# Kernel optimization log

Measured on AMD Instinct MI355X. Metric: run time of the kernel, lower is better.

Reference implementation:

```python
import jax, jax.numpy as jnp
import numpy as np

M = 16                      # multiplicity of each irrep block
INV3 = 1.0 / np.sqrt(3.0)   # w3j(1,1,0) component-normalized
INV2 = 1.0 / np.sqrt(2.0)   # w3j(1,1,1) component-normalized
A0 = 1.0 / np.sqrt(2.0 * M) # fan-in norm for 0e outputs (2 paths x mul 16)
A1 = 1.0 / np.sqrt(3.0 * M) # fan-in norm for 1o outputs (3 paths x mul 16)


def setup_inputs() -> dict:
    E, N, ED, HID = 100000, 10000, 32, 128
    WNUM = 2 * M * (2 * M) + 3 * M * M  # 1792 per-edge TP weights
    ks = jax.random.split(jax.random.key(0), 10)
    return {
        "dst": jax.random.randint(ks[0], (E,), 0, N),
        "x_src": jax.random.normal(ks[1], (E, 4 * M), jnp.float32),   # 16x0e+16x1o
        "x_dst": jax.random.normal(ks[2], (N, 4 * M), jnp.float32),
        "sh": jax.random.normal(ks[3], (E, 4), jnp.float32),          # 1x0e+1x1o
        "edge_attr": jax.random.normal(ks[4], (E, ED), jnp.float32),
        "We1": jax.random.normal(ks[5], (ED, HID), jnp.float32) / np.sqrt(ED),
        "be1": jnp.zeros((HID,), jnp.float32),
        "We2": jax.random.normal(ks[6], (HID, WNUM), jnp.float32) / np.sqrt(HID),
        "be2": jnp.zeros((WNUM,), jnp.float32),
        "Wr0": jax.random.normal(ks[7], (M, 2 * M), jnp.float32),     # 16x0e -> 32x0e
        "Wr1": jax.random.normal(ks[8], (M, M), jnp.float32),         # 16x1o -> 16x1o
    }


def _forward(dst, x_src, x_dst, sh, edge_attr, We1, be1, We2, be2, Wr0, Wr1):
    E = x_src.shape[0]
    N = x_dst.shape[0]
    o0 = 2 * M  # 32x0e tp output (scalars + gates)

    # edge MLP -> per-edge tensor-product weights [E, 1792]
    w = jax.nn.relu(edge_attr @ We1 + be1) @ We2 + be2
    i = 0
    w_ss = w[:, i:i + M * o0].reshape(E, M, o0); i += M * o0   # 0e x 0e -> 0e
    w_vv0 = w[:, i:i + M * o0].reshape(E, M, o0); i += M * o0  # 1o x 1o -> 0e
    w_sv = w[:, i:i + M * M].reshape(E, M, M); i += M * M      # 0e x 1o -> 1o
    w_vs = w[:, i:i + M * M].reshape(E, M, M); i += M * M      # 1o x 0e -> 1o
    w_vv1 = w[:, i:i + M * M].reshape(E, M, M)                 # 1o x 1o -> 1o

    s1 = x_src[:, :M]                       # [E, 16]
    v1 = x_src[:, M:].reshape(E, M, 3)      # [E, 16, 3]
    s2 = sh[:, 0]                           # [E]
    v2 = sh[:, 1:4]                         # [E, 3]

    # fully-connected tensor product with per-edge weights
    out0 = A0 * (jnp.einsum('em,emo->eo', s1 * s2[:, None], w_ss)
                 + INV3 * jnp.einsum('emc,ec,emo->eo', v1, v2, w_vv0))  # [E, 32]
    cross = jnp.cross(v1, v2[:, None, :])   # [E, 16, 3]
    out1 = A1 * (jnp.einsum('em,ec,emo->eoc', s1, v2, w_sv)
                 + jnp.einsum('emc,e,emo->eoc', v1, s2, w_vs)
                 + INV2 * jnp.einsum('emc,emo->eoc', cross, w_vv1))     # [E, 16, 3]
    msg = jnp.concatenate([out0, out1.reshape(E, -1)], axis=1)          # [E, 80]

    # scatter-mean over destination nodes
    ssum = jax.ops.segment_sum(msg, dst, num_segments=N)
    cnt = jax.ops.segment_sum(jnp.ones((E,), msg.dtype), dst, num_segments=N)
    msg = ssum / jnp.maximum(cnt, 1.0)[:, None]                          # [N, 80]

    # residual equivariant linear on x_dst
    sd = x_dst[:, :M]
    vd = x_dst[:, M:].reshape(N, M, 3)
    res0 = (sd @ Wr0) / np.sqrt(M)                                       # [N, 32]
    res1 = jnp.einsum('nmc,mo->noc', vd, Wr1) / np.sqrt(M)               # [N, 16, 3]
    msg = msg + jnp.concatenate([res0, res1.reshape(N, -1)], axis=1)

    # gate nonlinearity: relu(scalars), sigmoid(gates) * gated vectors
    scalars = jax.nn.relu(msg[:, :M])
    gates = jax.nn.sigmoid(msg[:, M:2 * M])
    gated = msg[:, 2 * M:].reshape(N, M, 3) * gates[:, :, None]
    return jnp.concatenate([scalars, gated.reshape(N, -1)], axis=1)      # [N, 64]


def reference(dst, x_src, x_dst, sh, edge_attr, We1, be1, We2, be2, Wr0, Wr1):
    return _forward(dst, x_src, x_dst, sh, edge_attr, We1, be1, We2, be2, Wr0, Wr1)
```

## Files before the change

### kernel.cpp

```cpp
#include <hip/hip_runtime.h>
#include <math.h>

#define WNUM 1792
#define HID 128

#define INV3C 0.5773502691896258f
#define INV2C 0.7071067811865476f
#define A0C   0.17677669529663687f
#define A1C   0.14433756729740643f

typedef short bf8 __attribute__((ext_vector_type(8)));
typedef _Float16 f16x8 __attribute__((ext_vector_type(8)));
typedef _Float16 f16x4 __attribute__((ext_vector_type(4)));
typedef float f32x4 __attribute__((ext_vector_type(4)));

__device__ inline unsigned short f2bf(float f) {
  union { float f; unsigned u; } v; v.f = f;
  unsigned r = v.u + 0x7FFFu + ((v.u >> 16) & 1u);
  return (unsigned short)(r >> 16);
}
__device__ inline float bf2f(unsigned short h) {
  union { unsigned u; float f; } v; v.u = ((unsigned)h) << 16;
  return v.f;
}
__device__ inline float wscale(int t) {
  if (t < 32) return A0C;
  if (t < 64) return A0C * INV3C;
  if (t < 96) return A1C;
  return A1C * INV2C;
}

__global__ __launch_bounds__(256) void prep_kernel(
    const float* __restrict__ We1, const float* __restrict__ We2,
    const float* __restrict__ be2,
    unsigned short* __restrict__ we1x, _Float16* __restrict__ we2h,
    float* __restrict__ be2p)
{
  int i = blockIdx.x * 256 + threadIdx.x;
  if (i < 28672) {
    int t = i >> 8, c = (i >> 6) & 3, lane = i & 63;
    int quad = lane >> 4, l15 = lane & 15;
    int col = t * 16 + l15;
    float sc = wscale(t);
    f16x8 v;
    #pragma unroll
    for (int j = 0; j < 8; ++j) {
      int k = c * 32 + quad * 8 + j;
      v[j] = (_Float16)(We2[(size_t)k * WNUM + col] * sc);
    }
    *(f16x8*)(we2h + (size_t)t * 2048 + c * 512 + lane * 8) = v;
  } else if (i < 29184) {
    int q = i - 28672;
    int c1 = q >> 6, lane = q & 63;
    int quad = lane >> 4, l15 = lane & 15;
    int col = c1 * 16 + l15;
    bf8 hh, ll;
    #pragma unroll
    for (int j = 0; j < 8; ++j) {
      int k = quad * 8 + j;
      float v = We1[k * HID + col];
      unsigned short hi = f2bf(v);
      hh[j] = (short)hi;
      ll[j] = (short)f2bf(v - bf2f(hi));
    }
    *(bf8*)(we1x + c1 * 1024 + lane * 8) = hh;
    *(bf8*)(we1x + c1 * 1024 + 512 + lane * 8) = ll;
  } else if (i < 30976) {
    int q = i - 29184;
    int t = q >> 4, l16 = q & 15;
    be2p[(t >> 1) * 32 + l16 * 2 + (t & 1)] = be2[q] * wscale(t);
  }
}

__device__ inline void chains2(const f16x8* a0, const f16x8* a1,
    f16x8 b0, f16x8 b1, f16x8 b2, f16x8 b3,
    f16x8 b4, f16x8 b5, f16x8 b6, f16x8 b7,
    float2 bias, f32x4* wa, f32x4* wb)
{
  f32x4 ca0 = {bias.x, bias.x, bias.x, bias.x};
  f32x4 cb0 = {bias.y, bias.y, bias.y, bias.y};
  f32x4 ca1 = ca0, cb1 = cb0;
  ca0 = __builtin_amdgcn_mfma_f32_16x16x32_f16(a0[0], b0, ca0, 0, 0, 0);
  cb0 = __builtin_amdgcn_mfma_f32_16x16x32_f16(a0[0], b4, cb0, 0, 0, 0);
  ca1 = __builtin_amdgcn_mfma_f32_16x16x32_f16(a1[0], b0, ca1, 0, 0, 0);
  cb1 = __builtin_amdgcn_mfma_f32_16x16x32_f16(a1[0], b4, cb1, 0, 0, 0);
  ca0 = __builtin_amdgcn_mfma_f32_16x16x32_f16(a0[1], b1, ca0, 0, 0, 0);
  cb0 = __builtin_amdgcn_mfma_f32_16x16x32_f16(a0[1], b5, cb0, 0, 0, 0);
  ca1 = __builtin_amdgcn_mfma_f32_16x16x32_f16(a1[1], b1, ca1, 0, 0, 0);
  cb1 = __builtin_amdgcn_mfma_f32_16x16x32_f16(a1[1], b5, cb1, 0, 0, 0);
  ca0 = __builtin_amdgcn_mfma_f32_16x16x32_f16(a0[2], b2, ca0, 0, 0, 0);
  cb0 = __builtin_amdgcn_mfma_f32_16x16x32_f16(a0[2], b6, cb0, 0, 0, 0);
  ca1 = __builtin_amdgcn_mfma_f32_16x16x32_f16(a1[2], b2, ca1, 0, 0, 0);
  cb1 = __builtin_amdgcn_mfma_f32_16x16x32_f16(a1[2], b6, cb1, 0, 0, 0);
  ca0 = __builtin_amdgcn_mfma_f32_16x16x32_f16(a0[3], b3, ca0, 0, 0, 0);
  cb0 = __builtin_amdgcn_mfma_f32_16x16x32_f16(a0[3], b7, cb0, 0, 0, 0);
  ca1 = __builtin_amdgcn_mfma_f32_16x16x32_f16(a1[3], b3, ca1, 0, 0, 0);
  cb1 = __builtin_amdgcn_mfma_f32_16x16x32_f16(a1[3], b7, cb1, 0, 0, 0);
  wa[0] = ca0; wb[0] = cb0; wa[1] = ca1; wb[1] = cb1;
}

#define LOADB(P) \
  f16x8 b0, b1, b2, b3, b4, b5, b6, b7; float2 bias2; \
  { const _Float16* q_ = bW + (size_t)(P) * 4096; \
    b0 = *(const f16x8*)(q_);        b1 = *(const f16x8*)(q_ + 512); \
    b2 = *(const f16x8*)(q_ + 1024); b3 = *(const f16x8*)(q_ + 1536); \
    b4 = *(const f16x8*)(q_ + 2048); b5 = *(const f16x8*)(q_ + 2560); \
    b6 = *(const f16x8*)(q_ + 3072); b7 = *(const f16x8*)(q_ + 3584); \
    bias2 = *(const float2*)(bp + (P) * 32); }

__global__ __launch_bounds__(128, 2) void edge_kernel(
    const float* __restrict__ ea, const float* __restrict__ xsrc,
    const float* __restrict__ sh, const int* __restrict__ dst,
    const float* __restrict__ be1,
    const unsigned short* __restrict__ we1x, const _Float16* __restrict__ we2h,
    const float* __restrict__ be2p,
    float* __restrict__ accn, float* __restrict__ cnt, int E)
{
  const int lane = threadIdx.x & 63;
  const int w    = threadIdx.x >> 6;
  const int quad = lane >> 4;
  const int l16  = lane & 15;
  const int eb   = (blockIdx.x * 2 + w) * 32;

  __shared__ _Float16 h_s[2][32][136];
  __shared__ _Float16 fss_s[2][16][32];
  __shared__ _Float16 fvv_s[2][16][32];
  __shared__ _Float16 s1h_s[2][16][32];
  __shared__ _Float16 v1h_s[2][16][3][32];
  __shared__ float4 vq_s[2][32];

  {
    int e2 = lane >> 1, mg = lane & 1;
    int ge = eb + e2;
    if (ge < E) {
      const float* xp = xsrc + (size_t)ge * 64;
      float4 sq0 = *(const float4*)(xp + mg * 8);
      float4 sq1 = *(const float4*)(xp + mg * 8 + 4);
      float s1a[8] = {sq0.x,sq0.y,sq0.z,sq0.w,sq1.x,sq1.y,sq1.z,sq1.w};
      const float* vp = xp + 16 + mg * 24;
      float la[24];
      #pragma unroll
      for (int qv = 0; qv < 6; ++qv) {
        float4 t = *(const float4*)(vp + qv * 4);
        la[qv*4+0] = t.x; la[qv*4+1] = t.y; la[qv*4+2] = t.z; la[qv*4+3] = t.w;
      }
      float4 shq = *(const float4*)(sh + (size_t)ge * 4);
      float s2 = shq.x, v2x = shq.y, v2y = shq.z, v2z = shq.w;
      #pragma unroll
      for (int mi = 0; mi < 8; ++mi) {
        int m = mg * 8 + mi;
        float v1x = la[mi*3], v1y = la[mi*3+1], v1z = la[mi*3+2];
        fss_s[w][m][e2] = (_Float16)(s1a[mi] * s2);
        fvv_s[w][m][e2] = (_Float16)(v1x*v2x + v1y*v2y + v1z*v2z);
        s1h_s[w][m][e2] = (_Float16)s1a[mi];
        v1h_s[w][m][0][e2] = (_Float16)v1x;
        v1h_s[w][m][1][e2] = (_Float16)v1y;
        v1h_s[w][m][2][e2] = (_Float16)v1z;
      }
      if (mg == 0) vq_s[w][e2] = make_float4(v2x, v2y, v2z, s2);
    } else {
      #pragma unroll
      for (int mi = 0; mi < 8; ++mi) {
        int m = mg * 8 + mi;
        fss_s[w][m][e2] = (_Float16)0.f;
        fvv_s[w][m][e2] = (_Float16)0.f;
        s1h_s[w][m][e2] = (_Float16)0.f;
        v1h_s[w][m][0][e2] = (_Float16)0.f;
        v1h_s[w][m][1][e2] = (_Float16)0.f;
        v1h_s[w][m][2][e2] = (_Float16)0.f;
      }
      if (mg == 0) vq_s[w][e2] = make_float4(0,0,0,0);
    }
  }

  {
    bf8 ah[2], al[2];
    #pragma unroll
    for (int g = 0; g < 2; ++g) {
      int gea = eb + g * 16 + l16; if (gea > E - 1) gea = E - 1;
      const float* ep = ea + (size_t)gea * 32 + quad * 8;
      float4 p0 = *(const float4*)ep;
      float4 p1 = *(const float4*)(ep + 4);
      float pv[8] = {p0.x,p0.y,p0.z,p0.w,p1.x,p1.y,p1.z,p1.w};
      #pragma unroll
      for (int j = 0; j < 8; ++j) {
        unsigned short hi = f2bf(pv[j]);
        ah[g][j] = (short)hi;
        al[g][j] = (short)f2bf(pv[j] - bf2f(hi));
      }
    }
    const unsigned short* wb1 = we1x + lane * 8;
    #pragma unroll 2
    for (int c = 0; c < 8; ++c) {
      bf8 bh = *(const bf8*)(wb1 + c * 1024);
      bf8 bl = *(const bf8*)(wb1 + c * 1024 + 512);
      float bias = be1[c * 16 + l16];
      #pragma unroll
      for (int g = 0; g < 2; ++g) {
        f32x4 hc = {bias, bias, bias, bias};
        hc = __builtin_amdgcn_mfma_f32_16x16x32_bf16(al[g], bh, hc, 0, 0, 0);
        hc = __builtin_amdgcn_mfma_f32_16x16x32_bf16(ah[g], bl, hc, 0, 0, 0);
        hc = __builtin_amdgcn_mfma_f32_16x16x32_bf16(ah[g], bh, hc, 0, 0, 0);
        #pragma unroll
        for (int r = 0; r < 4; ++r)
          h_s[w][g * 16 + quad * 4 + r][c * 16 + l16] = (_Float16)fmaxf(hc[r], 0.f);
      }
    }
  }
  __syncthreads();

  f16x8 af[2][4];
  #pragma unroll
  for (int g = 0; g < 2; ++g)
    #pragma unroll
    for (int ch = 0; ch < 4; ++ch)
      af[g][ch] = *(const f16x8*)&h_s[w][g * 16 + l16][ch * 32 + quad * 8];

  const _Float16* bW = we2h + lane * 8;
  const float* bp = be2p + l16 * 2;

  float m0a[2][4] = {{0,0,0,0},{0,0,0,0}}, m0b[2][4] = {{0,0,0,0},{0,0,0,0}};

  #pragma unroll 1
  for (int i = 0; i < 16; ++i) {
    LOADB(i)
    f32x4 wa[2], wb[2];
    chains2(af[0], af[1], b0,b1,b2,b3,b4,b5,b6,b7, bias2, wa, wb);
    #pragma unroll
    for (int g = 0; g < 2; ++g) {
      f16x4 fv = *(const f16x4*)&fss_s[w][i][g * 16 + quad * 4];
      #pragma unroll
      for (int r = 0; r < 4; ++r) {
        float f = (float)fv[r];
        m0a[g][r] = fmaf(wa[g][r], f, m0a[g][r]);
        m0b[g][r] = fmaf(wb[g][r], f, m0b[g][r]);
      }
    }
  }

  #pragma unroll 1
  for (int i = 0; i < 16; ++i) {
    LOADB(16 + i)
    f32x4 wa[2], wb[2];
    chains2(af[0], af[1], b0,b1,b2,b3,b4,b5,b6,b7, bias2, wa, wb);
    #pragma unroll
    for (int g = 0; g < 2; ++g) {
      f16x4 fv = *(const f16x4*)&fvv_s[w][i][g * 16 + quad * 4];
      #pragma unroll
      for (int r = 0; r < 4; ++r) {
        float f = (float)fv[r];
        m0a[g][r] = fmaf(wa[g][r], f, m0a[g][r]);
        m0b[g][r] = fmaf(wb[g][r], f, m0b[g][r]);
      }
    }
  }

  #pragma unroll
  for (int g = 0; g < 2; ++g)
    #pragma unroll
    for (int r = 0; r < 4; ++r) {
      int ge = eb + g * 16 + quad * 4 + r;
      if (ge < E) {
        float* ap = accn + (size_t)dst[ge] * 80;
        atomicAdd(ap + l16,      m0a[g][r]);
        atomicAdd(ap + 16 + l16, m0b[g][r]);
      }
    }
  if (lane < 32) {
    int ge = eb + lane;
    if (ge < E) atomicAdd(cnt + dst[ge], 1.0f);
  }

  float sg[2][4] = {{0,0,0,0},{0,0,0,0}};
  #pragma unroll 1
  for (int i = 0; i < 8; ++i) {
    LOADB(32 + i)
    f32x4 wa[2], wb[2];
    chains2(af[0], af[1], b0,b1,b2,b3,b4,b5,b6,b7, bias2, wa, wb);
    #pragma unroll
    for (int g = 0; g < 2; ++g) {
      f16x4 sA = *(const f16x4*)&s1h_s[w][2*i][g * 16 + quad * 4];
      f16x4 sB = *(const f16x4*)&s1h_s[w][2*i + 1][g * 16 + quad * 4];
      #pragma unroll
      for (int r = 0; r < 4; ++r)
        sg[g][r] = fmaf(wb[g][r], (float)sB[r], fmaf(wa[g][r], (float)sA[r], sg[g][r]));
    }
  }
  float4 vq[2][4];
  #pragma unroll
  for (int g = 0; g < 2; ++g)
    #pragma unroll
    for (int r = 0; r < 4; ++r) vq[g][r] = vq_s[w][g * 16 + quad * 4 + r];

  float m1x[2][4], m1y[2][4], m1z[2][4];
  #pragma unroll
  for (int g = 0; g < 2; ++g)
    #pragma unroll
    for (int r = 0; r < 4; ++r) {
      m1x[g][r] = sg[g][r] * vq[g][r].x;
      m1y[g][r] = sg[g][r] * vq[g][r].y;
      m1z[g][r] = sg[g][r] * vq[g][r].z;
    }

  {
    float ux[2][4] = {{0,0,0,0},{0,0,0,0}}, uy[2][4] = {{0,0,0,0},{0,0,0,0}},
          uz[2][4] = {{0,0,0,0},{0,0,0,0}};
    #pragma unroll 1
    for (int i = 0; i < 8; ++i) {
      LOADB(40 + i)
      f32x4 wa[2], wb[2];
      chains2(af[0], af[1], b0,b1,b2,b3,b4,b5,b6,b7, bias2, wa, wb);
      #pragma unroll
      for (int g = 0; g < 2; ++g) {
        f16x4 xA = *(const f16x4*)&v1h_s[w][2*i][0][g*16 + quad*4];
        f16x4 xB = *(const f16x4*)&v1h_s[w][2*i+1][0][g*16 + quad*4];
        f16x4 yA = *(const f16x4*)&v1h_s[w][2*i][1][g*16 + quad*4];
        f16x4 yB = *(const f16x4*)&v1h_s[w][2*i+1][1][g*16 + quad*4];
        f16x4 zA = *(const f16x4*)&v1h_s[w][2*i][2][g*16 + quad*4];
        f16x4 zB = *(const f16x4*)&v1h_s[w][2*i+1][2][g*16 + quad*4];
        #pragma unroll
        for (int r = 0; r < 4; ++r) {
          ux[g][r] = fmaf(wb[g][r], (float)xB[r], fmaf(wa[g][r], (float)xA[r], ux[g][r]));
          uy[g][r] = fmaf(wb[g][r], (float)yB[r], fmaf(wa[g][r], (float)yA[r], uy[g][r]));
          uz[g][r] = fmaf(wb[g][r], (float)zB[r], fmaf(wa[g][r], (float)zA[r], uz[g][r]));
        }
      }
    }
    #pragma unroll
    for (int g = 0; g < 2; ++g)
      #pragma unroll
      for (int r = 0; r < 4; ++r) {
        m1x[g][r] = fmaf(vq[g][r].w, ux[g][r], m1x[g][r]);
        m1y[g][r] = fmaf(vq[g][r].w, uy[g][r], m1y[g][r]);
        m1z[g][r] = fmaf(vq[g][r].w, uz[g][r], m1z[g][r]);
      }
  }

  {
    float ux[2][4] = {{0,0,0,0},{0,0,0,0}}, uy[2][4] = {{0,0,0,0},{0,0,0,0}},
          uz[2][4] = {{0,0,0,0},{0,0,0,0}};
    #pragma unroll 1
    for (int i = 0; i < 8; ++i) {
      LOADB(48 + i)
      f32x4 wa[2], wb[2];
      chains2(af[0], af[1], b0,b1,b2,b3,b4,b5,b6,b7, bias2, wa, wb);
      #pragma unroll
      for (int g = 0; g < 2; ++g) {
        f16x4 xA = *(const f16x4*)&v1h_s[w][2*i][0][g*16 + quad*4];
        f16x4 xB = *(const f16x4*)&v1h_s[w][2*i+1][0][g*16 + quad*4];
        f16x4 yA = *(const f16x4*)&v1h_s[w][2*i][1][g*16 + quad*4];
        f16x4 yB = *(const f16x4*)&v1h_s[w][2*i+1][1][g*16 + quad*4];
        f16x4 zA = *(const f16x4*)&v1h_s[w][2*i][2][g*16 + quad*4];
        f16x4 zB = *(const f16x4*)&v1h_s[w][2*i+1][2][g*16 + quad*4];
        #pragma unroll
        for (int r = 0; r < 4; ++r) {
          ux[g][r] = fmaf(wb[g][r], (float)xB[r], fmaf(wa[g][r], (float)xA[r], ux[g][r]));
          uy[g][r] = fmaf(wb[g][r], (float)yB[r], fmaf(wa[g][r], (float)yA[r], uy[g][r]));
          uz[g][r] = fmaf(wb[g][r], (float)zB[r], fmaf(wa[g][r], (float)zA[r], uz[g][r]));
        }
      }
    }
    #pragma unroll
    for (int g = 0; g < 2; ++g)
      #pragma unroll
      for (int r = 0; r < 4; ++r) {
        m1x[g][r] = fmaf(uy[g][r], vq[g][r].z, m1x[g][r]);
        m1x[g][r] = fmaf(-uz[g][r], vq[g][r].y, m1x[g][r]);
        m1y[g][r] = fmaf(uz[g][r], vq[g][r].x, m1y[g][r]);
        m1y[g][r] = fmaf(-ux[g][r], vq[g][r].z, m1y[g][r]);
        m1z[g][r] = fmaf(ux[g][r], vq[g][r].y, m1z[g][r]);
        m1z[g][r] = fmaf(-uy[g][r], vq[g][r].x, m1z[g][r]);
      }
  }

  #pragma unroll
  for (int g = 0; g < 2; ++g)
    #pragma unroll
    for (int r = 0; r < 4; ++r) {
      int ge = eb + g * 16 + quad * 4 + r;
      if (ge < E) {
        float* ap = accn + (size_t)dst[ge] * 80;
        atomicAdd(ap + 32 + l16*3 + 0, m1x[g][r]);
        atomicAdd(ap + 32 + l16*3 + 1, m1y[g][r]);
        atomicAdd(ap + 32 + l16*3 + 2, m1z[g][r]);
      }
    }
}

__global__ __launch_bounds__(256) void node_kernel(
    const float* __restrict__ accn, const float* __restrict__ cnt,
    const float* __restrict__ xdst, const float* __restrict__ Wr0,
    const float* __restrict__ Wr1, float* __restrict__ out, int N)
{
  int idx = blockIdx.x * 256 + threadIdx.x;
  int n = idx >> 6, j = idx & 63;
  if (n >= N) return;
  float inv = 1.0f / fmaxf(cnt[n], 1.0f);
  const float* ap = accn + (size_t)n * 80;
  const float* xd = xdst + (size_t)n * 64;
  float* op = out + (size_t)n * 64;
  if (j < 16) {
    float s = 0.f;
    #pragma unroll
    for (int m = 0; m < 16; ++m) s = fmaf(xd[m], Wr0[m * 32 + j], s);
    op[j] = fmaxf(ap[j] * inv + 0.25f * s, 0.f);
  } else {
    int jj = j - 16;
    int o = (jj * 86) >> 8;
    int c = jj - o * 3;
    float tg = 0.f, v = 0.f;
    #pragma unroll
    for (int m = 0; m < 16; ++m) {
      tg = fmaf(xd[m], Wr0[m * 32 + 16 + o], tg);
      v  = fmaf(xd[16 + m * 3 + c], Wr1[m * 16 + o], v);
    }
    float g = 1.0f / (1.0f + expf(-(ap[16 + o] * inv + 0.25f * tg)));
    op[16 + jj] = (ap[32 + jj] * inv + 0.25f * v) * g;
  }
}

extern "C" void kernel_launch(void* const* d_in, const int* in_sizes, int n_in,
                              void* d_out, int out_size, void* d_ws, size_t ws_size,
                              hipStream_t stream)
{
  const int*   dst  = (const int*)d_in[0];
  const float* xsrc = (const float*)d_in[1];
  const float* xdst = (const float*)d_in[2];
  const float* sh   = (const float*)d_in[3];
  const float* ea   = (const float*)d_in[4];
  const float* We1  = (const float*)d_in[5];
  const float* be1  = (const float*)d_in[6];
  const float* We2  = (const float*)d_in[7];
  const float* be2  = (const float*)d_in[8];
  const float* Wr0  = (const float*)d_in[9];
  const float* Wr1  = (const float*)d_in[10];
  const int E = in_sizes[0];
  const int N = in_sizes[2] / 64;

  char* ws = (char*)d_ws;
  _Float16* we2h = (_Float16*)ws;
  unsigned short* we1x = (unsigned short*)(ws + 458752);
  float* be2p = (float*)(ws + 475136);
  float* accn = (float*)(ws + 482560);
  float* cnt  = (float*)(ws + 482560 + (size_t)N * 320);

  hipMemsetAsync(accn, 0, (size_t)N * 320 + (size_t)N * 4, stream);

  prep_kernel<<<(30976 + 255) / 256, 256, 0, stream>>>(We1, We2, be2, we1x, we2h, be2p);
  edge_kernel<<<(E + 63) / 64, 128, 0, stream>>>(ea, xsrc, sh, dst, be1,
      we1x, we2h, be2p, accn, cnt, E);
  node_kernel<<<((size_t)N * 64 + 255) / 256, 256, 0, stream>>>(accn, cnt, xdst, Wr0, Wr1,
      (float*)d_out, N);
}
```

Baseline: 239.1 us.

## Stage We2 tiles into LDS with double-buffered global_load_lds shared by four waves

Each wave previously loaded its own copy of the per-edge MLP second-layer weight tiles straight from global memory. The block now has four waves, which cooperatively stream each 4096-element fp16 tile into a double-buffered LDS area with global_load_lds, prefetching the next tile while the current one is used. This cuts global/L2 traffic for the weights by sharing them across waves. In exchange it adds a block-wide barrier per tile and raises LDS use per block, which may lower occupancy.

After: 232.6 us. -2.7%, faster.

```diff
diff --git a/kernel.cpp b/kernel.cpp
--- a/kernel.cpp
+++ b/kernel.cpp
@@ -99,16 +99,17 @@
   wa[0] = ca0; wb[0] = cb0; wa[1] = ca1; wb[1] = cb1;
 }
 
-#define LOADB(P) \
-  f16x8 b0, b1, b2, b3, b4, b5, b6, b7; float2 bias2; \
-  { const _Float16* q_ = bW + (size_t)(P) * 4096; \
-    b0 = *(const f16x8*)(q_);        b1 = *(const f16x8*)(q_ + 512); \
-    b2 = *(const f16x8*)(q_ + 1024); b3 = *(const f16x8*)(q_ + 1536); \
-    b4 = *(const f16x8*)(q_ + 2048); b5 = *(const f16x8*)(q_ + 2560); \
-    b6 = *(const f16x8*)(q_ + 3072); b7 = *(const f16x8*)(q_ + 3584); \
-    bias2 = *(const float2*)(bp + (P) * 32); }
-
-__global__ __launch_bounds__(128, 2) void edge_kernel(
+#define LOADB_LDS(BASE) \
+  f16x8 b0 = *(const f16x8*)((BASE)); \
+  f16x8 b1 = *(const f16x8*)((BASE) + 512); \
+  f16x8 b2 = *(const f16x8*)((BASE) + 1024); \
+  f16x8 b3 = *(const f16x8*)((BASE) + 1536); \
+  f16x8 b4 = *(const f16x8*)((BASE) + 2048); \
+  f16x8 b5 = *(const f16x8*)((BASE) + 2560); \
+  f16x8 b6 = *(const f16x8*)((BASE) + 3072); \
+  f16x8 b7 = *(const f16x8*)((BASE) + 3584);
+
+__global__ __launch_bounds__(256, 2) void edge_kernel(
     const float* __restrict__ ea, const float* __restrict__ xsrc,
     const float* __restrict__ sh, const int* __restrict__ dst,
     const float* __restrict__ be1,
@@ -120,14 +121,25 @@
   const int w    = threadIdx.x >> 6;
   const int quad = lane >> 4;
   const int l16  = lane & 15;
-  const int eb   = (blockIdx.x * 2 + w) * 32;
-
-  __shared__ _Float16 h_s[2][32][136];
-  __shared__ _Float16 fss_s[2][16][32];
-  __shared__ _Float16 fvv_s[2][16][32];
-  __shared__ _Float16 s1h_s[2][16][32];
-  __shared__ _Float16 v1h_s[2][16][3][32];
-  __shared__ float4 vq_s[2][32];
+  const int eb   = (blockIdx.x * 4 + w) * 32;
+
+  __shared__ _Float16 Bsm[2][4096];
+  __shared__ _Float16 h_s[4][32][136];
+  __shared__ _Float16 fss_s[4][16][32];
+  __shared__ _Float16 fvv_s[4][16][32];
+  __shared__ _Float16 s1h_s[4][16][32];
+  __shared__ _Float16 v1h_s[4][16][3][32];
+  __shared__ float4 vq_s[4][32];
+
+  #define STAGEB(ldsbuf, p) { \
+    const _Float16* gsrc_ = we2h + (size_t)(p) * 4096; \
+    __builtin_amdgcn_global_load_lds( \
+      (const __attribute__((address_space(1))) void*)(gsrc_ + (w * 2) * 512 + lane * 8), \
+      (__attribute__((address_space(3))) void*)((ldsbuf) + (w * 2) * 512), 16, 0, 0); \
+    __builtin_amdgcn_global_load_lds( \
+      (const __attribute__((address_space(1))) void*)(gsrc_ + (w * 2 + 1) * 512 + lane * 8), \
+      (__attribute__((address_space(3))) void*)((ldsbuf) + (w * 2 + 1) * 512), 16, 0, 0); \
+  }
 
   {
     int e2 = lane >> 1, mg = lane & 1;
@@ -178,6 +190,7 @@
     #pragma unroll
     for (int g = 0; g < 2; ++g) {
       int gea = eb + g * 16 + l16; if (gea > E - 1) gea = E - 1;
+      if (gea < 0) gea = 0;
       const float* ep = ea + (size_t)gea * 32 + quad * 8;
       float4 p0 = *(const float4*)ep;
       float4 p1 = *(const float4*)(ep + 4);
@@ -207,6 +220,8 @@
       }
     }
   }
+
+  STAGEB(&Bsm[0][0], 0)
   __syncthreads();
 
   f16x8 af[2][4];
@@ -216,14 +231,17 @@
     for (int ch = 0; ch < 4; ++ch)
       af[g][ch] = *(const f16x8*)&h_s[w][g * 16 + l16][ch * 32 + quad * 8];
 
-  const _Float16* bW = we2h + lane * 8;
   const float* bp = be2p + l16 * 2;
 
   float m0a[2][4] = {{0,0,0,0},{0,0,0,0}}, m0b[2][4] = {{0,0,0,0},{0,0,0,0}};
+  int p = 0;
 
   #pragma unroll 1
   for (int i = 0; i < 16; ++i) {
-    LOADB(i)
+    STAGEB(&Bsm[(p + 1) & 1][0], p + 1)
+    const _Float16* bL = &Bsm[p & 1][lane * 8];
+    LOADB_LDS(bL)
+    float2 bias2 = *(const float2*)(bp + p * 32);
     f32x4 wa[2], wb[2];
     chains2(af[0], af[1], b0,b1,b2,b3,b4,b5,b6,b7, bias2, wa, wb);
     #pragma unroll
@@ -236,11 +254,16 @@
         m0b[g][r] = fmaf(wb[g][r], f, m0b[g][r]);
       }
     }
+    __syncthreads();
+    ++p;
   }
 
   #pragma unroll 1
   for (int i = 0; i < 16; ++i) {
-    LOADB(16 + i)
+    STAGEB(&Bsm[(p + 1) & 1][0], p + 1)
+    const _Float16* bL = &Bsm[p & 1][lane * 8];
+    LOADB_LDS(bL)
+    float2 bias2 = *(const float2*)(bp + p * 32);
     f32x4 wa[2], wb[2];
     chains2(af[0], af[1], b0,b1,b2,b3,b4,b5,b6,b7, bias2, wa, wb);
     #pragma unroll
@@ -253,6 +276,8 @@
         m0b[g][r] = fmaf(wb[g][r], f, m0b[g][r]);
       }
     }
+    __syncthreads();
+    ++p;
   }
 
   #pragma unroll
@@ -274,7 +299,10 @@
   float sg[2][4] = {{0,0,0,0},{0,0,0,0}};
   #pragma unroll 1
   for (int i = 0; i < 8; ++i) {
-    LOADB(32 + i)
+    STAGEB(&Bsm[(p + 1) & 1][0], p + 1)
+    const _Float16* bL = &Bsm[p & 1][lane * 8];
+    LOADB_LDS(bL)
+    float2 bias2 = *(const float2*)(bp + p * 32);
     f32x4 wa[2], wb[2];
     chains2(af[0], af[1], b0,b1,b2,b3,b4,b5,b6,b7, bias2, wa, wb);
     #pragma unroll
@@ -285,6 +313,8 @@
       for (int r = 0; r < 4; ++r)
         sg[g][r] = fmaf(wb[g][r], (float)sB[r], fmaf(wa[g][r], (float)sA[r], sg[g][r]));
     }
+    __syncthreads();
+    ++p;
   }
   float4 vq[2][4];
   #pragma unroll
@@ -307,7 +337,10 @@
           uz[2][4] = {{0,0,0,0},{0,0,0,0}};
     #pragma unroll 1
     for (int i = 0; i < 8; ++i) {
-      LOADB(40 + i)
+      STAGEB(&Bsm[(p + 1) & 1][0], p + 1)
+      const _Float16* bL = &Bsm[p & 1][lane * 8];
+      LOADB_LDS(bL)
+      float2 bias2 = *(const float2*)(bp + p * 32);
       f32x4 wa[2], wb[2];
       chains2(af[0], af[1], b0,b1,b2,b3,b4,b5,b6,b7, bias2, wa, wb);
       #pragma unroll
@@ -325,6 +358,8 @@
           uz[g][r] = fmaf(wb[g][r], (float)zB[r], fmaf(wa[g][r], (float)zA[r], uz[g][r]));
         }
       }
+      __syncthreads();
+      ++p;
     }
     #pragma unroll
     for (int g = 0; g < 2; ++g)
@@ -341,7 +376,10 @@
           uz[2][4] = {{0,0,0,0},{0,0,0,0}};
     #pragma unroll 1
     for (int i = 0; i < 8; ++i) {
-      LOADB(48 + i)
+      if (p + 1 < 56) STAGEB(&Bsm[(p + 1) & 1][0], p + 1)
+      const _Float16* bL = &Bsm[p & 1][lane * 8];
+      LOADB_LDS(bL)
+      float2 bias2 = *(const float2*)(bp + p * 32);
       f32x4 wa[2], wb[2];
       chains2(af[0], af[1], b0,b1,b2,b3,b4,b5,b6,b7, bias2, wa, wb);
       #pragma unroll
@@ -359,6 +397,8 @@
           uz[g][r] = fmaf(wb[g][r], (float)zB[r], fmaf(wa[g][r], (float)zA[r], uz[g][r]));
         }
       }
+      __syncthreads();
+      ++p;
     }
     #pragma unroll
     for (int g = 0; g < 2; ++g)
@@ -385,6 +425,7 @@
         atomicAdd(ap + 32 + l16*3 + 2, m1z[g][r]);
       }
     }
+  #undef STAGEB
 }
 
 __global__ __launch_bounds__(256) void node_kernel(
@@ -447,7 +488,7 @@
   hipMemsetAsync(accn, 0, (size_t)N * 320 + (size_t)N * 4, stream);
 
   prep_kernel<<<(30976 + 255) / 256, 256, 0, stream>>>(We1, We2, be2, we1x, we2h, be2p);
-  edge_kernel<<<(E + 63) / 64, 128, 0, stream>>>(ea, xsrc, sh, dst, be1,
+  edge_kernel<<<(E + 127) / 128, 256, 0, stream>>>(ea, xsrc, sh, dst, be1,
       we1x, we2h, be2p, accn, cnt, E);
   node_kernel<<<((size_t)N * 64 + 255) / 256, 256, 0, stream>>>(accn, cnt, xdst, Wr0, Wr1,
       (float*)d_out, N);
```
